# Kernel tuning notes

Hardware: AMD Instinct MI355X
Metric: run time of the kernel (lower is better)

Reference implementation:

```python
import jax, jax.numpy as jnp
import numpy as np

V, T, D, H, DK = 16, 2048, 64, 128, 48
LONGEST_GAP, TIME_WINDOW = 144, 48
N_ROLE = 2 * V * V + V


def _run_lengths(md):
    Tn = md.shape[-1]
    m = np.stack((md, md[:, ::-1]), 0).astype(np.int64)
    m[:, :, 0] = 1 - m[:, :, 0]
    for i in range(Tn - 1):
        m[:, :, i + 1] = (1 - m[:, :, i + 1]) * (1 + m[:, :, i])
    return m[0], m[1][:, ::-1].copy()


def _tree_depth_np(mask, times):
    # faithful numpy port of the cached branch of _compute_tree_depth
    Vn, Tn = mask.shape
    time_ind = np.argsort(times, axis=-1)
    time_rev = np.argsort(time_ind, axis=-1)
    mask_depth = np.take_along_axis(mask.astype(np.int64), time_ind, -1)
    current_depth = 1
    max_depth = np.zeros_like(mask_depth)
    prev_mask = np.zeros_like(max_depth)
    next_mask = np.zeros_like(max_depth)
    prev_values = np.zeros_like(max_depth)
    next_values = np.zeros_like(max_depth)
    mask_depth_copy = mask_depth.copy()
    mask_l, mask_r = _run_lengths(mask_depth)
    ci = np.tile(np.arange(Tn), (Vn, 1))
    max_ind = Tn - 1
    while (mask_l + mask_r - 1).max() > LONGEST_GAP:
        centers = mask_l == LONGEST_GAP
        left_ind = mask_l >= LONGEST_GAP
        right_ind = (mask_r + mask_l - 1 >= LONGEST_GAP) & (mask_l <= LONGEST_GAP)
        next_mask[centers] = ((ci + mask_r) > max_ind)[centers].astype(np.int64)
        prev_values[centers] = ci[centers] - mask_l[centers]
        next_values[centers] = (ci[centers] + mask_r[centers]) * (1 - next_mask[centers])
        current_depth += 1
        current_val = mask_l + mask_r
        mask_l[left_ind] -= LONGEST_GAP
        mask_r[right_ind] -= (current_val - LONGEST_GAP)[right_ind]
        mask_r[centers] = 0
        mask_depth_copy[centers] = 1
    mask_depth = mask_depth_copy
    if (1 - mask_depth[:, -1]).sum() > 0 or (1 - mask_depth[:, 0]).sum() > 0:
        end_indices = mask_depth[:, -1] == 0
        start_indices = mask_depth[:, 0] == 0
        prev_mask[:, 0] = start_indices
        next_mask[:, -1] = end_indices
        first_hist = np.arange(Tn, 0, -1)
        last_hist = np.arange(Tn)
        first_hist = np.argmax(first_hist[None, :] * mask_depth, -1)
        last_hist = np.argmax(last_hist[None, :] * mask_depth, -1)
        next_values[start_indices, 0] = first_hist[start_indices]
        prev_values[end_indices, -1] = last_hist[end_indices]
        mask_depth[:, 0] = 1
        mask_depth[:, -1] = 1
        max_depth[end_indices, -1] += current_depth
        max_depth[start_indices, 0] += current_depth
        current_depth += 1
    mask_l, mask_r = _run_lengths(mask_depth)
    while mask_l.sum() > 0:
        half = (mask_l + mask_r) // 2
        centers = (half == mask_l) & (half > 0)
        max_depth[centers] += current_depth
        prev_values[centers] = ci[centers] - mask_l[centers]
        next_values[centers] = ci[centers] + mask_r[centers]
        current_depth += 1
        odd = (mask_l + mask_r + 1) % 2
        s1 = mask_l >= half
        mask_l[s1] -= half[s1]
        s2 = (mask_r > half - odd) & (half > 0)
        mask_r[s2] -= (half - odd)[s2] + 1
    window_indices = ci - TIME_WINDOW
    window_mask = (window_indices < 0) | (window_indices > max_ind)
    window_mask[:, TIME_WINDOW:] |= max_depth[:, TIME_WINDOW:] > max_depth[:, :-TIME_WINDOW]
    window_mask = window_mask.astype(np.int64)
    window_indices = np.clip(window_indices, 0, max_ind)
    max_depth_f = np.take_along_axis(max_depth, time_rev, -1).astype(np.float32)
    next_mask_f = np.take_along_axis(next_mask, time_rev, -1).astype(np.float32)
    prev_mask_f = np.take_along_axis(prev_mask, time_rev, -1).astype(np.float32)
    window_mask_f = np.take_along_axis(window_mask, time_rev, -1).astype(np.float32)
    pv = np.take_along_axis(time_ind, np.clip(prev_values, 0, max_ind), -1)
    pv = np.take_along_axis(pv, time_rev, -1)
    nv = np.take_along_axis(time_ind, np.clip(next_values, 0, max_ind), -1)
    nv = np.take_along_axis(nv, time_rev, -1)
    wi = np.take_along_axis(time_ind, window_indices, -1)
    wi = np.take_along_axis(wi, time_rev, -1)
    offsets = Tn * np.arange(Vn)[:, None]
    indices = np.arange(Tn)[None, :] + offsets
    pv = pv + offsets
    nv = nv + offsets
    wi = wi + offsets
    max_depth_f = max_depth_f + time_ind / 2.0 / (2.0 * Tn)
    return dict(max_depth=max_depth_f, prev_values=pv, next_values=nv, indices=indices,
                prev_mask=prev_mask_f, next_mask=next_mask_f, window_indices=wi,
                window_mask=window_mask_f)


def _mlp(x, W1, b1, W2, b2):
    return jax.nn.relu(x @ W1 + b1) @ W2 + b2


def _forward(encoded, u, Wq1, bq1, Wq2, bq2, Wk1, bk1, Wk2, bk2, Wv1, bv1, Wv2, bv2,
             role_emb, Wd1, bd1, Wd2, bd2, Wm1, bm1, Wm2, bm2,
             prev_values, next_values, window_indices, indices,
             prev_mask, next_mask, window_mask, max_depth):
    Vn, Tn = max_depth.shape
    N = Vn * Tn
    enc = encoded[0].reshape(N, -1)  # [N, D]
    uv = u[0].reshape(N)
    # per-forward depth jitter (torch: max_depth += rand_like/2/(2T))
    md = max_depth + jax.random.uniform(jax.random.key(42), max_depth.shape, max_depth.dtype) / (4.0 * Tn)
    comp = md[:, :, None] > md.T[None]  # [V, T, V]: query deeper than key -> key conditioned on
    pv = jnp.broadcast_to(prev_values.T[None], (Vn, Tn, Vn))
    nv = jnp.where(comp, indices.T[None], next_values.T[None])
    base = Vn * jnp.arange(Vn, dtype=jnp.int32)[:, None] + jnp.arange(Vn, dtype=jnp.int32)[None, :]
    prev_role = jnp.broadcast_to(base[:, None, :], (Vn, Tn, Vn))
    next_role = Vn * Vn + prev_role
    window_role = 2 * Vn * Vn + jnp.broadcast_to(jnp.arange(Vn, dtype=jnp.int32)[:, None, None], (Vn, Tn, 1))
    valid_prev = jnp.broadcast_to((prev_mask.T == 0.0)[None], (Vn, Tn, Vn))
    valid_next = jnp.logical_or(comp, (next_mask.T == 0.0)[None])
    valid_win = (window_mask == 0.0)[:, :, None]
    K = 2 * Vn + 1
    nbr = jnp.concatenate([pv, nv, window_indices[:, :, None]], -1).reshape(N, K)
    roles = jnp.concatenate([prev_role, next_role, window_role], -1).reshape(N, K)
    valid = jnp.concatenate([valid_prev, valid_next, valid_win], -1).reshape(N, K)
    q = _mlp(enc, Wq1, bq1, Wq2, bq2)  # [N, DK]
    k = _mlp(enc, Wk1, bk1, Wk2, bk2)
    v = _mlp(enc, Wv1, bv1, Wv2, bv2)
    keys = k[nbr] + role_emb[roles]  # [N, K, DK] irregular gather
    vals = v[nbr]
    scores = jnp.einsum('nd,nkd->nk', q, keys) / jnp.sqrt(jnp.asarray(q.shape[-1], q.dtype))
    attn = jax.nn.softmax(jnp.where(valid, scores, -1e9), axis=-1)
    ctx = jnp.einsum('nk,nkd->nd', attn, vals)
    dp = _mlp(jnp.concatenate([enc, ctx], -1), Wd1, bd1, Wd2, bd2)  # copula dist params
    mp = _mlp(enc, Wm1, bm1, Wm2, bm2)  # marginal params

    def nlogp(x, mu, log_s):
        s = jax.nn.softplus(log_s) + 1e-3
        z = (x - mu) / s
        return 0.5 * z * z + jnp.log(s) + 0.5 * jnp.log(2.0 * jnp.pi)

    nll = nlogp(uv, dp[:, 0], dp[:, 1]) + nlogp(uv, mp[:, 0], mp[:, 1])
    return nll.reshape(Vn, Tn)


def setup_inputs() -> dict:
    rng = np.random.default_rng(0)
    times = np.sort(rng.uniform(size=(V, T)).astype(np.float32), axis=-1)
    mask = np.zeros((V, T), dtype=bool)
    mask[:, : T // 2] = True  # observed history / prediction gap > longest_gap
    c = _tree_depth_np(mask, times)
    key = jax.random.key(0)
    ks = jax.random.split(key, 13)

    def lin(k, din, dout):
        return jax.random.normal(k, (din, dout), jnp.float32) / np.sqrt(din)

    return {
        'encoded': jax.random.normal(ks[0], (1, V, T, D), jnp.float32),
        'u': jax.random.uniform(ks[1], (1, V, T), jnp.float32),
        'Wq1': lin(ks[2], D, H), 'bq1': jnp.zeros(H, jnp.float32),
        'Wq2': lin(ks[3], H, DK), 'bq2': jnp.zeros(DK, jnp.float32),
        'Wk1': lin(ks[4], D, H), 'bk1': jnp.zeros(H, jnp.float32),
        'Wk2': lin(ks[5], H, DK), 'bk2': jnp.zeros(DK, jnp.float32),
        'Wv1': lin(ks[6], D, H), 'bv1': jnp.zeros(H, jnp.float32),
        'Wv2': lin(ks[7], H, DK), 'bv2': jnp.zeros(DK, jnp.float32),
        'role_emb': 0.02 * jax.random.normal(ks[8], (N_ROLE, DK), jnp.float32),
        'Wd1': lin(ks[9], D + DK, H), 'bd1': jnp.zeros(H, jnp.float32),
        'Wd2': lin(ks[10], H, 2), 'bd2': jnp.zeros(2, jnp.float32),
        'Wm1': lin(ks[11], D, H), 'bm1': jnp.zeros(H, jnp.float32),
        'Wm2': lin(ks[12], H, 2), 'bm2': jnp.zeros(2, jnp.float32),
        'prev_values': jnp.asarray(c['prev_values'], jnp.int32),
        'next_values': jnp.asarray(c['next_values'], jnp.int32),
        'window_indices': jnp.asarray(c['window_indices'], jnp.int32),
        'indices': jnp.asarray(c['indices'], jnp.int32),
        'prev_mask': jnp.asarray(c['prev_mask'], jnp.float32),
        'next_mask': jnp.asarray(c['next_mask'], jnp.float32),
        'window_mask': jnp.asarray(c['window_mask'], jnp.float32),
        'max_depth': jnp.asarray(c['max_depth'], jnp.float32),
    }


def reference(encoded, u, Wq1, bq1, Wq2, bq2, Wk1, bk1, Wk2, bk2, Wv1, bv1, Wv2, bv2,
              role_emb, Wd1, bd1, Wd2, bd2, Wm1, bm1, Wm2, bm2,
              prev_values, next_values, window_indices, indices,
              prev_mask, next_mask, window_mask, max_depth):
    return _forward(encoded, u, Wq1, bq1, Wq2, bq2, Wk1, bk1, Wk2, bk2, Wv1, bv1, Wv2, bv2,
                    role_emb, Wd1, bd1, Wd2, bd2, Wm1, bm1, Wm2, bm2,
                    prev_values, next_values, window_indices, indices,
                    prev_mask, next_mask, window_mask, max_depth)
```

## Files before the change

kernel.cpp:

```cpp
#include <hip/hip_runtime.h>
#include <math.h>

#define VN 16
#define TN 2048
#define NROWS (VN*TN)
#define DIN 64
#define HID 128
#define DKD 48
#define KNB 33
#define BR64 64
#define BRH 32
#define XPAD 68
#define HPAD 66
#define XPADH 36
#define SPAD 52
#define RQW 528

__device__ __forceinline__ unsigned rotl32(unsigned x, int d){ return (x<<d)|(x>>(32-d)); }

__device__ __forceinline__ void tf2x32(unsigned c0, unsigned c1, unsigned& y0, unsigned& y1){
  const unsigned k0 = 0u, k1 = 42u;
  const unsigned k2 = k0 ^ k1 ^ 0x1BD11BDAu;
  unsigned x0 = c0, x1 = c1;
  x0 += k0; x1 += k1;
#define TF_R(r) { x0 += x1; x1 = rotl32(x1,(r)); x1 ^= x0; }
  TF_R(13) TF_R(15) TF_R(26) TF_R(6)   x0 += k1; x1 += k2 + 1u;
  TF_R(17) TF_R(29) TF_R(16) TF_R(24)  x0 += k2; x1 += k0 + 2u;
  TF_R(13) TF_R(15) TF_R(26) TF_R(6)   x0 += k0; x1 += k1 + 3u;
  TF_R(17) TF_R(29) TF_R(16) TF_R(24)  x0 += k1; x1 += k2 + 4u;
  TF_R(13) TF_R(15) TF_R(26) TF_R(6)   x0 += k2; x1 += k0 + 5u;
#undef TF_R
  y0 = x0; y1 = x1;
}

__device__ __forceinline__ double md64_of(const float* __restrict__ max_depth, int n){
  unsigned y0, y1;
  tf2x32(0u, (unsigned)n, y0, y1);
  unsigned long long bits = (((unsigned long long)y0) << 32) | (unsigned long long)y1;
  unsigned long long fb = (bits >> 12) | 0x3FF0000000000000ull;
  double f; __builtin_memcpy(&f, &fb, 8);
  f -= 1.0;
  return (double)max_depth[n] + f * (1.0/8192.0);
}

__global__ __launch_bounds__(256) void prep_kernel(const float* __restrict__ max_depth,
    const int* __restrict__ pv, const int* __restrict__ nv,
    const float* __restrict__ pm, const float* __restrict__ nm,
    const int* __restrict__ wi, const float* __restrict__ wm,
    double* __restrict__ mdT, int* __restrict__ pvT, int* __restrict__ nvT,
    float* __restrict__ pmT, float* __restrict__ nmT,
    int* __restrict__ wiT, float* __restrict__ wmT)
{
  int n = blockIdx.x*256 + threadIdx.x;
  int v = n >> 11, t = n & 2047;
  int o = t*VN + v;
  mdT[o]  = md64_of(max_depth, n);
  pvT[o]  = pv[n];
  nvT[o]  = nv[n];
  pmT[o]  = pm[n];
  nmT[o]  = nm[n];
  wiT[o]  = wi[n];
  wmT[o]  = wm[n];
}

__global__ __launch_bounds__(256) void rq_kernel(const float* __restrict__ q,
    const float* __restrict__ role_emb, float* __restrict__ rqT)
{
  __shared__ __align__(16) float s_R[KNB][SPAD];
  __shared__ __align__(16) float s_Q[64][SPAD];
  int tid = threadIdx.x;
  int v  = blockIdx.x >> 5;
  int tc = blockIdx.x & 31;
  int t0 = tc*64;

  for (int idx = tid; idx < KNB*DKD; idx += 256){
    int j = idx / DKD, d = idx - j*DKD;
    int role = (j<16) ? (v*16+j) : ((j<32) ? 256+v*16+(j-16) : 512+v);
    s_R[j][d] = role_emb[(size_t)role*DKD + d];
  }
  for (int idx = tid; idx < 64*DKD; idx += 256){
    int r = idx / DKD, d = idx - r*DKD;
    s_Q[r][d] = q[((size_t)v*TN + t0 + r)*DKD + d];
  }
  __syncthreads();

  int r = tid & 63, p = tid >> 6;
  int t = t0 + r;
  for (int j = p; j < KNB; j += 4){
    float acc = 0.0f;
    #pragma unroll
    for (int d4=0; d4<12; d4++){
      const float4 qq = *reinterpret_cast<const float4*>(&s_Q[r][4*d4]);
      const float4 rr = *reinterpret_cast<const float4*>(&s_R[j][4*d4]);
      acc = fmaf(qq.x, rr.x, acc);
      acc = fmaf(qq.y, rr.y, acc);
      acc = fmaf(qq.z, rr.z, acc);
      acc = fmaf(qq.w, rr.w, acc);
    }
    rqT[(size_t)t*RQW + v*KNB + j] = acc;
  }
}

__global__ __launch_bounds__(256) void qkv_kernel(const float* __restrict__ enc,
    const float* __restrict__ Wq1, const float* __restrict__ bq1,
    const float* __restrict__ Wq2, const float* __restrict__ bq2,
    const float* __restrict__ Wk1, const float* __restrict__ bk1,
    const float* __restrict__ Wk2, const float* __restrict__ bk2,
    const float* __restrict__ Wv1, const float* __restrict__ bv1,
    const float* __restrict__ Wv2, const float* __restrict__ bv2,
    float* __restrict__ qo, float* __restrict__ ko, float* __restrict__ vo)
{
  __shared__ __align__(16) float s_x[DIN][XPAD];
  __shared__ __align__(16) float s_h[HID][HPAD];
  int tid = threadIdx.x;
  int mm   = blockIdx.x / 512;
  int base = (blockIdx.x - mm*512) * BR64;

  const float *W1, *b1, *W2, *b2; float* outp;
  if (mm == 0){ W1=Wq1; b1=bq1; W2=Wq2; b2=bq2; outp=qo; }
  else if (mm == 1){ W1=Wk1; b1=bk1; W2=Wk2; b2=bk2; outp=ko; }
  else        { W1=Wv1; b1=bv1; W2=Wv2; b2=bv2; outp=vo; }

  for (int idx = tid; idx < BR64*DIN; idx += 256){
    int r = idx >> 6, c = idx & 63;
    s_x[c][r] = enc[(size_t)(base+r)*DIN + c];
  }
  __syncthreads();

  const int u0 = (tid & 31) * 4;
  const int r0 = (tid >> 5) * 8;
  {
    float acc[8][4];
    float c0=b1[u0], c1=b1[u0+1], c2=b1[u0+2], c3=b1[u0+3];
    #pragma unroll
    for (int r=0;r<8;r++){ acc[r][0]=c0; acc[r][1]=c1; acc[r][2]=c2; acc[r][3]=c3; }
    #pragma unroll 8
    for (int i=0;i<DIN;i++){
      const float4 xa = *reinterpret_cast<const float4*>(&s_x[i][r0]);
      const float4 xb = *reinterpret_cast<const float4*>(&s_x[i][r0+4]);
      const float4 wv = *reinterpret_cast<const float4*>(&W1[i*HID + u0]);
      float xd[8] = {xa.x, xa.y, xa.z, xa.w, xb.x, xb.y, xb.z, xb.w};
      float wd[4] = {wv.x, wv.y, wv.z, wv.w};
      #pragma unroll
      for (int r=0;r<8;r++)
        #pragma unroll
        for (int j=0;j<4;j++)
          acc[r][j] = fmaf(xd[r], wd[j], acc[r][j]);
    }
    #pragma unroll
    for (int j=0;j<4;j++){
      float4 h0, h1;
      h0.x=fmaxf(acc[0][j],0.0f); h0.y=fmaxf(acc[1][j],0.0f);
      h0.z=fmaxf(acc[2][j],0.0f); h0.w=fmaxf(acc[3][j],0.0f);
      h1.x=fmaxf(acc[4][j],0.0f); h1.y=fmaxf(acc[5][j],0.0f);
      h1.z=fmaxf(acc[6][j],0.0f); h1.w=fmaxf(acc[7][j],0.0f);
      *reinterpret_cast<float4*>(&s_h[u0+j][r0])   = h0;
      *reinterpret_cast<float4*>(&s_h[u0+j][r0+4]) = h1;
    }
  }
  __syncthreads();

  const int uo0 = (tid & 15) * 3;
  const int rr0 = (tid >> 4) * 4;
  {
    float a[4][3];
    float c0=b2[uo0], c1=b2[uo0+1], c2=b2[uo0+2];
    #pragma unroll
    for (int r=0;r<4;r++){ a[r][0]=c0; a[r][1]=c1; a[r][2]=c2; }
    #pragma unroll 8
    for (int i=0;i<HID;i++){
      const float4 hv = *reinterpret_cast<const float4*>(&s_h[i][rr0]);
      float w0 = W2[i*DKD+uo0], w1 = W2[i*DKD+uo0+1], w2 = W2[i*DKD+uo0+2];
      float hd[4] = {hv.x, hv.y, hv.z, hv.w};
      #pragma unroll
      for (int r=0;r<4;r++){
        a[r][0]=fmaf(hd[r],w0,a[r][0]);
        a[r][1]=fmaf(hd[r],w1,a[r][1]);
        a[r][2]=fmaf(hd[r],w2,a[r][2]);
      }
    }
    #pragma unroll
    for (int r=0;r<4;r++){
      float* op = outp + (size_t)(base+rr0+r)*DKD;
      op[uo0]=a[r][0]; op[uo0+1]=a[r][1]; op[uo0+2]=a[r][2];
    }
  }
}

__global__ __launch_bounds__(256) void attn_kernel(const float* __restrict__ qv,
    const float* __restrict__ kv, const float* __restrict__ vv,
    const double* __restrict__ mdT,
    const int* __restrict__ pvT, const int* __restrict__ nvT,
    const float* __restrict__ pmT, const float* __restrict__ nmT,
    const int* __restrict__ wiT, const float* __restrict__ wmT,
    const float* __restrict__ rqT,
    float* __restrict__ ctx_out)
{
  __shared__ __align__(16) float s_K[64][SPAD];
  __shared__ __align__(16) float s_V[64][SPAD];
  __shared__ __align__(16) float s_Q[16][SPAD];
  __shared__ float s_rq[16][34];
  __shared__ int    s_g[64];
  __shared__ double s_md[16];
  __shared__ float  s_pm[16], s_nm[16], s_wm[16];
  __shared__ float  s_P1[16][17], s_P2i[16][17], s_P2n[16][17], s_pw[16];

  int tid = threadIdx.x;
  int t = blockIdx.x;
  int mbase = t*VN;

  if (tid < 64){
    int c = tid & 15, g;
    if (tid < 16)      g = pvT[mbase + c];
    else if (tid < 32) g = c*TN + t;
    else if (tid < 48) g = nvT[mbase + c];
    else               g = wiT[mbase + c];
    s_g[tid] = g;
  } else if (tid < 80){
    s_md[tid-64] = mdT[mbase + (tid-64)];
  } else if (tid < 96){
    s_pm[tid-80] = pmT[mbase + (tid-80)];
  } else if (tid < 112){
    s_nm[tid-96] = nmT[mbase + (tid-96)];
  } else if (tid < 128){
    s_wm[tid-112] = wmT[mbase + (tid-112)];
  }
  for (int idx = tid; idx < 16*DKD; idx += 256){
    int v = idx / DKD, d = idx - v*DKD;
    s_Q[v][d] = qv[((size_t)v*TN + t)*DKD + d];
  }
  for (int idx = tid; idx < RQW; idx += 256){
    int v = idx / KNB, j = idx - v*KNB;
    s_rq[v][j] = rqT[(size_t)t*RQW + idx];
  }
  __syncthreads();
  for (int idx = tid; idx < 64*DKD; idx += 256){
    int slot = idx / DKD, d = idx - slot*DKD;
    size_t off = (size_t)s_g[slot]*DKD + d;
    s_K[slot][d] = kv[off];
    s_V[slot][d] = vv[off];
  }
  __syncthreads();

  const int v = tid >> 4, j = tid & 15;
  float a1=0.f, a2=0.f, a3=0.f;
  #pragma unroll
  for (int d4=0; d4<12; d4++){
    const float4 qq = *reinterpret_cast<const float4*>(&s_Q[v][4*d4]);
    const float4 kp = *reinterpret_cast<const float4*>(&s_K[j][4*d4]);
    const float4 ki = *reinterpret_cast<const float4*>(&s_K[16+j][4*d4]);
    const float4 kn = *reinterpret_cast<const float4*>(&s_K[32+j][4*d4]);
    a1=fmaf(qq.x,kp.x,a1); a1=fmaf(qq.y,kp.y,a1); a1=fmaf(qq.z,kp.z,a1); a1=fmaf(qq.w,kp.w,a1);
    a2=fmaf(qq.x,ki.x,a2); a2=fmaf(qq.y,ki.y,a2); a2=fmaf(qq.z,ki.z,a2); a2=fmaf(qq.w,ki.w,a2);
    a3=fmaf(qq.x,kn.x,a3); a3=fmaf(qq.y,kn.y,a3); a3=fmaf(qq.z,kn.z,a3); a3=fmaf(qq.w,kn.w,a3);
  }
  float aw = 0.f;
  if (j == 0){
    #pragma unroll
    for (int d4=0; d4<12; d4++){
      const float4 qq = *reinterpret_cast<const float4*>(&s_Q[v][4*d4]);
      const float4 kw = *reinterpret_cast<const float4*>(&s_K[48+v][4*d4]);
      aw=fmaf(qq.x,kw.x,aw); aw=fmaf(qq.y,kw.y,aw); aw=fmaf(qq.z,kw.z,aw); aw=fmaf(qq.w,kw.w,aw);
    }
  }
  const bool comp = s_md[v] > s_md[j];
  float scP = (a1 + s_rq[v][j]) / 6.928203230275509f;
  if (s_pm[j] != 0.0f) scP = -1e9f;
  float scN = ((comp ? a2 : a3) + s_rq[v][16+j]) / 6.928203230275509f;
  if (!(comp || s_nm[j] == 0.0f)) scN = -1e9f;
  float scW = -1e9f;
  if (j == 0){
    scW = (aw + s_rq[v][32]) / 6.928203230275509f;
    if (s_wm[v] != 0.0f) scW = -1e9f;
  }
  float m = fmaxf(scP, scN);
  if (j == 0) m = fmaxf(m, scW);
  #pragma unroll
  for (int o=1;o<=8;o<<=1) m = fmaxf(m, __shfl_xor(m, o, 64));
  float eP = expf(scP - m), eN = expf(scN - m);
  float eW = (j == 0) ? expf(scW - m) : 0.0f;
  float S = eP + eN + eW;
  #pragma unroll
  for (int o=1;o<=8;o<<=1) S += __shfl_xor(S, o, 64);
  s_P1 [v][j] = eP / S;
  s_P2i[v][j] = comp ? (eN / S) : 0.0f;
  s_P2n[v][j] = comp ? 0.0f : (eN / S);
  if (j == 0) s_pw[v] = eW / S;
  __syncthreads();

  if (tid < 192){
    int pvr = tid / 12, d4 = tid % 12;
    float4 c; c.x=0.f; c.y=0.f; c.z=0.f; c.w=0.f;
    #pragma unroll 4
    for (int jj=0; jj<16; jj++){
      float p = s_P1[pvr][jj];
      const float4 vp = *reinterpret_cast<const float4*>(&s_V[jj][4*d4]);
      c.x=fmaf(p,vp.x,c.x); c.y=fmaf(p,vp.y,c.y); c.z=fmaf(p,vp.z,c.z); c.w=fmaf(p,vp.w,c.w);
    }
    #pragma unroll 4
    for (int jj=0; jj<16; jj++){
      float pi = s_P2i[pvr][jj], pn = s_P2n[pvr][jj];
      const float4 vi = *reinterpret_cast<const float4*>(&s_V[16+jj][4*d4]);
      const float4 vn = *reinterpret_cast<const float4*>(&s_V[32+jj][4*d4]);
      c.x=fmaf(pi,vi.x,c.x); c.y=fmaf(pi,vi.y,c.y); c.z=fmaf(pi,vi.z,c.z); c.w=fmaf(pi,vi.w,c.w);
      c.x=fmaf(pn,vn.x,c.x); c.y=fmaf(pn,vn.y,c.y); c.z=fmaf(pn,vn.z,c.z); c.w=fmaf(pn,vn.w,c.w);
    }
    {
      float p = s_pw[pvr];
      const float4 vw = *reinterpret_cast<const float4*>(&s_V[48+pvr][4*d4]);
      c.x=fmaf(p,vw.x,c.x); c.y=fmaf(p,vw.y,c.y); c.z=fmaf(p,vw.z,c.z); c.w=fmaf(p,vw.w,c.w);
    }
    *reinterpret_cast<float4*>(&ctx_out[((size_t)pvr*TN + t)*DKD + 4*d4]) = c;
  }
}

__device__ __forceinline__ double nlogp_d(double x, double mu, double ls){
  double sp = fmax(ls, 0.0) + log1p(exp(-fabs(ls)));
  double s = sp + 1e-3;
  double z = (x - mu) / s;
  return 0.5*z*z + log(s) + 0.9189385332046727417803297;
}

__global__ __launch_bounds__(256) void heads_kernel(const float* __restrict__ enc,
    const float* __restrict__ ctx, const float* __restrict__ uu,
    const float* __restrict__ Wd1, const float* __restrict__ bd1,
    const float* __restrict__ Wd2, const float* __restrict__ bd2,
    const float* __restrict__ Wm1, const float* __restrict__ bm1,
    const float* __restrict__ Wm2, const float* __restrict__ bm2,
    float* __restrict__ out)
{
  __shared__ __align__(16) float s_x[DIN+DKD][XPADH];
  __shared__ float s_o[BRH][4];
  int tid = threadIdx.x;
  int base = blockIdx.x * BRH;

  for (int idx = tid; idx < BRH*DIN; idx += 256){
    int r = idx >> 6, c = idx & 63;
    s_x[c][r] = enc[(size_t)(base+r)*DIN + c];
  }
  for (int idx = tid; idx < BRH*DKD; idx += 256){
    int r = idx / DKD, c = idx - r*DKD;
    s_x[DIN + c][r] = ctx[(size_t)(base+r)*DKD + c];
  }
  __syncthreads();

  const int u0 = (tid & 31) * 4;
  const int r0 = (tid >> 5) * 4;

  float pd[4][2] = {{0,0},{0,0},{0,0},{0,0}};
  float pm[4][2] = {{0,0},{0,0},{0,0},{0,0}};

  {
    float acc[4][4];
    float c0=bd1[u0], c1=bd1[u0+1], c2=bd1[u0+2], c3=bd1[u0+3];
    #pragma unroll
    for (int r=0;r<4;r++){ acc[r][0]=c0; acc[r][1]=c1; acc[r][2]=c2; acc[r][3]=c3; }
    #pragma unroll 8
    for (int i=0;i<DIN+DKD;i++){
      const float4 xv = *reinterpret_cast<const float4*>(&s_x[i][r0]);
      const float4 wv = *reinterpret_cast<const float4*>(&Wd1[i*HID + u0]);
      float xd[4] = {xv.x, xv.y, xv.z, xv.w};
      float wd[4] = {wv.x, wv.y, wv.z, wv.w};
      #pragma unroll
      for (int r=0;r<4;r++)
        #pragma unroll
        for (int j=0;j<4;j++)
          acc[r][j] = fmaf(xd[r], wd[j], acc[r][j]);
    }
    #pragma unroll
    for (int j=0;j<4;j++){
      const float2 w2 = *reinterpret_cast<const float2*>(&Wd2[(u0+j)*2]);
      #pragma unroll
      for (int r=0;r<4;r++){
        float h = fmaxf(acc[r][j], 0.0f);
        pd[r][0] = fmaf(h, w2.x, pd[r][0]);
        pd[r][1] = fmaf(h, w2.y, pd[r][1]);
      }
    }
  }
  {
    float acc[4][4];
    float c0=bm1[u0], c1=bm1[u0+1], c2=bm1[u0+2], c3=bm1[u0+3];
    #pragma unroll
    for (int r=0;r<4;r++){ acc[r][0]=c0; acc[r][1]=c1; acc[r][2]=c2; acc[r][3]=c3; }
    #pragma unroll 8
    for (int i=0;i<DIN;i++){
      const float4 xv = *reinterpret_cast<const float4*>(&s_x[i][r0]);
      const float4 wv = *reinterpret_cast<const float4*>(&Wm1[i*HID + u0]);
      float xd[4] = {xv.x, xv.y, xv.z, xv.w};
      float wd[4] = {wv.x, wv.y, wv.z, wv.w};
      #pragma unroll
      for (int r=0;r<4;r++)
        #pragma unroll
        for (int j=0;j<4;j++)
          acc[r][j] = fmaf(xd[r], wd[j], acc[r][j]);
    }
    #pragma unroll
    for (int j=0;j<4;j++){
      const float2 w2 = *reinterpret_cast<const float2*>(&Wm2[(u0+j)*2]);
      #pragma unroll
      for (int r=0;r<4;r++){
        float h = fmaxf(acc[r][j], 0.0f);
        pm[r][0] = fmaf(h, w2.x, pm[r][0]);
        pm[r][1] = fmaf(h, w2.y, pm[r][1]);
      }
    }
  }
  #pragma unroll
  for (int o=1;o<=16;o<<=1){
    #pragma unroll
    for (int r=0;r<4;r++){
      pd[r][0]+=__shfl_xor(pd[r][0],o,64); pd[r][1]+=__shfl_xor(pd[r][1],o,64);
      pm[r][0]+=__shfl_xor(pm[r][0],o,64); pm[r][1]+=__shfl_xor(pm[r][1],o,64);
    }
  }
  if ((tid & 31) == 0){
    #pragma unroll
    for (int r=0;r<4;r++){
      s_o[r0+r][0] = pd[r][0] + bd2[0];
      s_o[r0+r][1] = pd[r][1] + bd2[1];
      s_o[r0+r][2] = pm[r][0] + bm2[0];
      s_o[r0+r][3] = pm[r][1] + bm2[1];
    }
  }
  __syncthreads();

  if (tid < BRH){
    double x = (double)uu[base + tid];
    out[base + tid] = (float)(nlogp_d(x, (double)s_o[tid][0], (double)s_o[tid][1]) +
                              nlogp_d(x, (double)s_o[tid][2], (double)s_o[tid][3]));
  }
}

extern "C" void kernel_launch(void* const* d_in, const int* in_sizes, int n_in,
                              void* d_out, int out_size, void* d_ws, size_t ws_size,
                              hipStream_t stream) {
  const float* encoded = (const float*)d_in[0];
  const float* u       = (const float*)d_in[1];
  const float* Wq1 = (const float*)d_in[2];  const float* bq1 = (const float*)d_in[3];
  const float* Wq2 = (const float*)d_in[4];  const float* bq2 = (const float*)d_in[5];
  const float* Wk1 = (const float*)d_in[6];  const float* bk1 = (const float*)d_in[7];
  const float* Wk2 = (const float*)d_in[8];  const float* bk2 = (const float*)d_in[9];
  const float* Wv1 = (const float*)d_in[10]; const float* bv1 = (const float*)d_in[11];
  const float* Wv2 = (const float*)d_in[12]; const float* bv2 = (const float*)d_in[13];
  const float* role_emb = (const float*)d_in[14];
  const float* Wd1 = (const float*)d_in[15]; const float* bd1 = (const float*)d_in[16];
  const float* Wd2 = (const float*)d_in[17]; const float* bd2 = (const float*)d_in[18];
  const float* Wm1 = (const float*)d_in[19]; const float* bm1 = (const float*)d_in[20];
  const float* Wm2 = (const float*)d_in[21]; const float* bm2 = (const float*)d_in[22];
  const int*   prev_values    = (const int*)d_in[23];
  const int*   next_values    = (const int*)d_in[24];
  const int*   window_indices = (const int*)d_in[25];
  const float* prev_mask   = (const float*)d_in[27];
  const float* next_mask   = (const float*)d_in[28];
  const float* window_mask = (const float*)d_in[29];
  const float* max_depth   = (const float*)d_in[30];
  float* out = (float*)d_out;

  double* mdT = (double*)d_ws;
  float* q  = (float*)(mdT + NROWS);
  float* k  = q  + (size_t)NROWS*DKD;
  float* v  = k  + (size_t)NROWS*DKD;
  float* cx = v  + (size_t)NROWS*DKD;
  int*   pvT  = (int*)(cx + (size_t)NROWS*DKD);
  int*   nvT  = pvT + NROWS;
  float* pmT  = (float*)(nvT + NROWS);
  float* nmT  = pmT + NROWS;
  int*   wiT  = (int*)(nmT + NROWS);
  float* wmT  = (float*)(wiT + NROWS);
  float* rqT  = wmT + NROWS;

  prep_kernel<<<NROWS/256, 256, 0, stream>>>(max_depth,
      prev_values, next_values, prev_mask, next_mask, window_indices, window_mask,
      mdT, pvT, nvT, pmT, nmT, wiT, wmT);
  qkv_kernel<<<3*(NROWS/BR64), 256, 0, stream>>>(encoded,
      Wq1,bq1,Wq2,bq2, Wk1,bk1,Wk2,bk2, Wv1,bv1,Wv2,bv2, q, k, v);
  rq_kernel<<<512, 256, 0, stream>>>(q, role_emb, rqT);
  attn_kernel<<<TN, 256, 0, stream>>>(q, k, v, mdT,
      pvT, nvT, pmT, nmT, wiT, wmT, rqT, cx);
  heads_kernel<<<NROWS/BRH, 256, 0, stream>>>(encoded, cx, u,
      Wd1,bd1,Wd2,bd2, Wm1,bm1,Wm2,bm2, out);
}
```

Before: 138.5 us.

## Split heads into per-MLP blocks with 64-row tiles and separate NLL kernel

The fused heads kernel, which ran both MLP heads serially on 32-row tiles, is replaced by a head_kernel. It launches separate blocks for the duration and mark MLPs, each on 64-row tiles with an 8x4 register tile, and writes the 2-wide outputs to workspace. A small nll_kernel then computes the double-precision log-likelihood. Separately, the QKV first-layer register tiling changes from 8 rows x 4 units to 4 rows x 8 units. The heads change aims for more parallelism and register reuse, at the cost of an extra launch, an extra workspace round trip, and re-reading the encoded input twice.

```diff
diff --git a/kernel.cpp b/kernel.cpp
--- a/kernel.cpp
+++ b/kernel.cpp
@@ -9,10 +9,8 @@
 #define DKD 48
 #define KNB 33
 #define BR64 64
-#define BRH 32
 #define XPAD 68
 #define HPAD 66
-#define XPADH 36
 #define SPAD 52
 #define RQW 528
 
@@ -127,35 +125,35 @@
   }
   __syncthreads();
 
-  const int u0 = (tid & 31) * 4;
-  const int r0 = (tid >> 5) * 8;
+  const int u0 = (tid & 15) * 8;
+  const int r0 = (tid >> 4) * 4;
   {
-    float acc[8][4];
-    float c0=b1[u0], c1=b1[u0+1], c2=b1[u0+2], c3=b1[u0+3];
-    #pragma unroll
-    for (int r=0;r<8;r++){ acc[r][0]=c0; acc[r][1]=c1; acc[r][2]=c2; acc[r][3]=c3; }
+    float acc[4][8];
+    #pragma unroll
+    for (int j=0;j<8;j++){
+      float b = b1[u0+j];
+      #pragma unroll
+      for (int r=0;r<4;r++) acc[r][j] = b;
+    }
     #pragma unroll 8
     for (int i=0;i<DIN;i++){
-      const float4 xa = *reinterpret_cast<const float4*>(&s_x[i][r0]);
-      const float4 xb = *reinterpret_cast<const float4*>(&s_x[i][r0+4]);
-      const float4 wv = *reinterpret_cast<const float4*>(&W1[i*HID + u0]);
-      float xd[8] = {xa.x, xa.y, xa.z, xa.w, xb.x, xb.y, xb.z, xb.w};
-      float wd[4] = {wv.x, wv.y, wv.z, wv.w};
+      const float4 xv = *reinterpret_cast<const float4*>(&s_x[i][r0]);
+      const float4 wa = *reinterpret_cast<const float4*>(&W1[i*HID + u0]);
+      const float4 wb = *reinterpret_cast<const float4*>(&W1[i*HID + u0 + 4]);
+      float xd[4] = {xv.x, xv.y, xv.z, xv.w};
+      float wd[8] = {wa.x, wa.y, wa.z, wa.w, wb.x, wb.y, wb.z, wb.w};
       #pragma unroll
-      for (int r=0;r<8;r++)
+      for (int r=0;r<4;r++)
         #pragma unroll
-        for (int j=0;j<4;j++)
+        for (int j=0;j<8;j++)
           acc[r][j] = fmaf(xd[r], wd[j], acc[r][j]);
     }
     #pragma unroll
-    for (int j=0;j<4;j++){
-      float4 h0, h1;
-      h0.x=fmaxf(acc[0][j],0.0f); h0.y=fmaxf(acc[1][j],0.0f);
-      h0.z=fmaxf(acc[2][j],0.0f); h0.w=fmaxf(acc[3][j],0.0f);
-      h1.x=fmaxf(acc[4][j],0.0f); h1.y=fmaxf(acc[5][j],0.0f);
-      h1.z=fmaxf(acc[6][j],0.0f); h1.w=fmaxf(acc[7][j],0.0f);
-      *reinterpret_cast<float4*>(&s_h[u0+j][r0])   = h0;
-      *reinterpret_cast<float4*>(&s_h[u0+j][r0+4]) = h1;
+    for (int j=0;j<8;j++){
+      float4 hv;
+      hv.x=fmaxf(acc[0][j],0.0f); hv.y=fmaxf(acc[1][j],0.0f);
+      hv.z=fmaxf(acc[2][j],0.0f); hv.w=fmaxf(acc[3][j],0.0f);
+      *reinterpret_cast<float4*>(&s_h[u0+j][r0]) = hv;
     }
   }
   __syncthreads();
@@ -314,6 +312,86 @@
   }
 }
 
+__global__ __launch_bounds__(256) void head_kernel(const float* __restrict__ enc,
+    const float* __restrict__ ctx,
+    const float* __restrict__ Wd1, const float* __restrict__ bd1,
+    const float* __restrict__ Wd2, const float* __restrict__ bd2,
+    const float* __restrict__ Wm1, const float* __restrict__ bm1,
+    const float* __restrict__ Wm2, const float* __restrict__ bm2,
+    float* __restrict__ dpo, float* __restrict__ mpo)
+{
+  __shared__ __align__(16) float s_x[DIN+DKD][XPAD];
+  int tid = threadIdx.x;
+  int mode = blockIdx.x >> 9;
+  int base = (blockIdx.x & 511) * BR64;
+
+  const float *W1, *b1, *W2, *b2; float* outp; int nin;
+  if (mode == 0){ W1=Wd1; b1=bd1; W2=Wd2; b2=bd2; outp=dpo; nin=DIN+DKD; }
+  else          { W1=Wm1; b1=bm1; W2=Wm2; b2=bm2; outp=mpo; nin=DIN; }
+
+  for (int idx = tid; idx < BR64*DIN; idx += 256){
+    int r = idx >> 6, c = idx & 63;
+    s_x[c][r] = enc[(size_t)(base+r)*DIN + c];
+  }
+  if (mode == 0){
+    for (int idx = tid; idx < BR64*DKD; idx += 256){
+      int r = idx / DKD, c = idx - r*DKD;
+      s_x[DIN + c][r] = ctx[(size_t)(base+r)*DKD + c];
+    }
+  }
+  __syncthreads();
+
+  const int u0 = (tid & 31) * 4;
+  const int r0 = (tid >> 5) * 8;
+
+  float pp[8][2] = {{0,0},{0,0},{0,0},{0,0},{0,0},{0,0},{0,0},{0,0}};
+  {
+    float acc[8][4];
+    float c0=b1[u0], c1=b1[u0+1], c2=b1[u0+2], c3=b1[u0+3];
+    #pragma unroll
+    for (int r=0;r<8;r++){ acc[r][0]=c0; acc[r][1]=c1; acc[r][2]=c2; acc[r][3]=c3; }
+    #pragma unroll 8
+    for (int i=0;i<nin;i++){
+      const float4 xa = *reinterpret_cast<const float4*>(&s_x[i][r0]);
+      const float4 xb = *reinterpret_cast<const float4*>(&s_x[i][r0+4]);
+      const float4 wv = *reinterpret_cast<const float4*>(&W1[i*HID + u0]);
+      float xd[8] = {xa.x, xa.y, xa.z, xa.w, xb.x, xb.y, xb.z, xb.w};
+      float wd[4] = {wv.x, wv.y, wv.z, wv.w};
+      #pragma unroll
+      for (int r=0;r<8;r++)
+        #pragma unroll
+        for (int j=0;j<4;j++)
+          acc[r][j] = fmaf(xd[r], wd[j], acc[r][j]);
+    }
+    #pragma unroll
+    for (int j=0;j<4;j++){
+      const float2 w2 = *reinterpret_cast<const float2*>(&W2[(u0+j)*2]);
+      #pragma unroll
+      for (int r=0;r<8;r++){
+        float h = fmaxf(acc[r][j], 0.0f);
+        pp[r][0] = fmaf(h, w2.x, pp[r][0]);
+        pp[r][1] = fmaf(h, w2.y, pp[r][1]);
+      }
+    }
+  }
+  #pragma unroll
+  for (int o=1;o<=16;o<<=1){
+    #pragma unroll
+    for (int r=0;r<8;r++){
+      pp[r][0]+=__shfl_xor(pp[r][0],o,64);
+      pp[r][1]+=__shfl_xor(pp[r][1],o,64);
+    }
+  }
+  if ((tid & 31) == 0){
+    float b20 = b2[0], b21 = b2[1];
+    #pragma unroll
+    for (int r=0;r<8;r++){
+      outp[(size_t)(base+r0+r)*2    ] = pp[r][0] + b20;
+      outp[(size_t)(base+r0+r)*2 + 1] = pp[r][1] + b21;
+    }
+  }
+}
+
 __device__ __forceinline__ double nlogp_d(double x, double mu, double ls){
   double sp = fmax(ls, 0.0) + log1p(exp(-fabs(ls)));
   double s = sp + 1e-3;
@@ -321,115 +399,13 @@
   return 0.5*z*z + log(s) + 0.9189385332046727417803297;
 }
 
-__global__ __launch_bounds__(256) void heads_kernel(const float* __restrict__ enc,
-    const float* __restrict__ ctx, const float* __restrict__ uu,
-    const float* __restrict__ Wd1, const float* __restrict__ bd1,
-    const float* __restrict__ Wd2, const float* __restrict__ bd2,
-    const float* __restrict__ Wm1, const float* __restrict__ bm1,
-    const float* __restrict__ Wm2, const float* __restrict__ bm2,
-    float* __restrict__ out)
-{
-  __shared__ __align__(16) float s_x[DIN+DKD][XPADH];
-  __shared__ float s_o[BRH][4];
-  int tid = threadIdx.x;
-  int base = blockIdx.x * BRH;
-
-  for (int idx = tid; idx < BRH*DIN; idx += 256){
-    int r = idx >> 6, c = idx & 63;
-    s_x[c][r] = enc[(size_t)(base+r)*DIN + c];
-  }
-  for (int idx = tid; idx < BRH*DKD; idx += 256){
-    int r = idx / DKD, c = idx - r*DKD;
-    s_x[DIN + c][r] = ctx[(size_t)(base+r)*DKD + c];
-  }
-  __syncthreads();
-
-  const int u0 = (tid & 31) * 4;
-  const int r0 = (tid >> 5) * 4;
-
-  float pd[4][2] = {{0,0},{0,0},{0,0},{0,0}};
-  float pm[4][2] = {{0,0},{0,0},{0,0},{0,0}};
-
-  {
-    float acc[4][4];
-    float c0=bd1[u0], c1=bd1[u0+1], c2=bd1[u0+2], c3=bd1[u0+3];
-    #pragma unroll
-    for (int r=0;r<4;r++){ acc[r][0]=c0; acc[r][1]=c1; acc[r][2]=c2; acc[r][3]=c3; }
-    #pragma unroll 8
-    for (int i=0;i<DIN+DKD;i++){
-      const float4 xv = *reinterpret_cast<const float4*>(&s_x[i][r0]);
-      const float4 wv = *reinterpret_cast<const float4*>(&Wd1[i*HID + u0]);
-      float xd[4] = {xv.x, xv.y, xv.z, xv.w};
-      float wd[4] = {wv.x, wv.y, wv.z, wv.w};
-      #pragma unroll
-      for (int r=0;r<4;r++)
-        #pragma unroll
-        for (int j=0;j<4;j++)
-          acc[r][j] = fmaf(xd[r], wd[j], acc[r][j]);
-    }
-    #pragma unroll
-    for (int j=0;j<4;j++){
-      const float2 w2 = *reinterpret_cast<const float2*>(&Wd2[(u0+j)*2]);
-      #pragma unroll
-      for (int r=0;r<4;r++){
-        float h = fmaxf(acc[r][j], 0.0f);
-        pd[r][0] = fmaf(h, w2.x, pd[r][0]);
-        pd[r][1] = fmaf(h, w2.y, pd[r][1]);
-      }
-    }
-  }
-  {
-    float acc[4][4];
-    float c0=bm1[u0], c1=bm1[u0+1], c2=bm1[u0+2], c3=bm1[u0+3];
-    #pragma unroll
-    for (int r=0;r<4;r++){ acc[r][0]=c0; acc[r][1]=c1; acc[r][2]=c2; acc[r][3]=c3; }
-    #pragma unroll 8
-    for (int i=0;i<DIN;i++){
-      const float4 xv = *reinterpret_cast<const float4*>(&s_x[i][r0]);
-      const float4 wv = *reinterpret_cast<const float4*>(&Wm1[i*HID + u0]);
-      float xd[4] = {xv.x, xv.y, xv.z, xv.w};
-      float wd[4] = {wv.x, wv.y, wv.z, wv.w};
-      #pragma unroll
-      for (int r=0;r<4;r++)
-        #pragma unroll
-        for (int j=0;j<4;j++)
-          acc[r][j] = fmaf(xd[r], wd[j], acc[r][j]);
-    }
-    #pragma unroll
-    for (int j=0;j<4;j++){
-      const float2 w2 = *reinterpret_cast<const float2*>(&Wm2[(u0+j)*2]);
-      #pragma unroll
-      for (int r=0;r<4;r++){
-        float h = fmaxf(acc[r][j], 0.0f);
-        pm[r][0] = fmaf(h, w2.x, pm[r][0]);
-        pm[r][1] = fmaf(h, w2.y, pm[r][1]);
-      }
-    }
-  }
-  #pragma unroll
-  for (int o=1;o<=16;o<<=1){
-    #pragma unroll
-    for (int r=0;r<4;r++){
-      pd[r][0]+=__shfl_xor(pd[r][0],o,64); pd[r][1]+=__shfl_xor(pd[r][1],o,64);
-      pm[r][0]+=__shfl_xor(pm[r][0],o,64); pm[r][1]+=__shfl_xor(pm[r][1],o,64);
-    }
-  }
-  if ((tid & 31) == 0){
-    #pragma unroll
-    for (int r=0;r<4;r++){
-      s_o[r0+r][0] = pd[r][0] + bd2[0];
-      s_o[r0+r][1] = pd[r][1] + bd2[1];
-      s_o[r0+r][2] = pm[r][0] + bm2[0];
-      s_o[r0+r][3] = pm[r][1] + bm2[1];
-    }
-  }
-  __syncthreads();
-
-  if (tid < BRH){
-    double x = (double)uu[base + tid];
-    out[base + tid] = (float)(nlogp_d(x, (double)s_o[tid][0], (double)s_o[tid][1]) +
-                              nlogp_d(x, (double)s_o[tid][2], (double)s_o[tid][3]));
-  }
+__global__ __launch_bounds__(256) void nll_kernel(const float* __restrict__ uu,
+    const float* __restrict__ dpo, const float* __restrict__ mpo, float* __restrict__ out)
+{
+  int n = blockIdx.x*256 + threadIdx.x;
+  double x = (double)uu[n];
+  out[n] = (float)(nlogp_d(x, (double)dpo[2*n], (double)dpo[2*n+1]) +
+                   nlogp_d(x, (double)mpo[2*n], (double)mpo[2*n+1]));
 }
 
 extern "C" void kernel_launch(void* const* d_in, const int* in_sizes, int n_in,
@@ -469,6 +445,8 @@
   int*   wiT  = (int*)(nmT + NROWS);
   float* wmT  = (float*)(wiT + NROWS);
   float* rqT  = wmT + NROWS;
+  float* dpo  = rqT + (size_t)TN*RQW;
+  float* mpo  = dpo + 2*NROWS;
 
   prep_kernel<<<NROWS/256, 256, 0, stream>>>(max_depth,
       prev_values, next_values, prev_mask, next_mask, window_indices, window_mask,
@@ -478,6 +456,7 @@
   rq_kernel<<<512, 256, 0, stream>>>(q, role_emb, rqT);
   attn_kernel<<<TN, 256, 0, stream>>>(q, k, v, mdT,
       pvT, nvT, pmT, nmT, wiT, wmT, rqT, cx);
-  heads_kernel<<<NROWS/BRH, 256, 0, stream>>>(encoded, cx, u,
-      Wd1,bd1,Wd2,bd2, Wm1,bm1,Wm2,bm2, out);
-}
+  head_kernel<<<2*512, 256, 0, stream>>>(encoded, cx,
+      Wd1,bd1,Wd2,bd2, Wm1,bm1,Wm2,bm2, dpo, mpo);
+  nll_kernel<<<NROWS/256, 256, 0, stream>>>(u, dpo, mpo, out);
+}
```

New measurement: 139.6 us. No clear change (+0.8%).
